# Performance work log

Measured on AMD Instinct MI355X. Metric: run time of the kernel, lower is better.

## Reference

```python
import jax, jax.numpy as jnp
import numpy as np

D_MODEL = 1024
N_HEADS = 16
D_HIDDEN = 4096
EPS = 1e-6
SCALE = float(np.sqrt(D_MODEL // N_HEADS))


def setup_inputs() -> dict:
    key = jax.random.key(0)
    ks = jax.random.split(key, 12)
    d, h = D_MODEL, D_HIDDEN
    init = lambda k, shape, fan_in: jax.random.uniform(k, shape, jnp.float32, -1.0, 1.0) / np.sqrt(fan_in)
    return {
        "x": jax.random.normal(ks[0], (2, 2048, d), jnp.float32),
        "W_q": init(ks[1], (d, d), d),
        "W_k": init(ks[2], (d, d), d),
        "W_v": init(ks[3], (d, d), d),
        "W_o": init(ks[4], (d, d), d),
        "b_o": init(ks[5], (d,), d),
        "attn_norm_w": 1.0 + jax.random.normal(ks[6], (d,), jnp.float32) / np.sqrt(d),
        "ffn_norm_w": 1.0 + jax.random.normal(ks[7], (d,), jnp.float32) / np.sqrt(d),
        "W_gate": init(ks[8], (d, h), d),
        "W_hidden": init(ks[9], (d, h), d),
        "W_out": init(ks[10], (h, d), h),
        "b_out": init(ks[11], (d,), h),
    }


def rmsnorm(x, w):
    return w * x * jax.lax.rsqrt(jnp.mean(x * x, axis=-1, keepdims=True) + EPS)


def attention(x, W_q, W_k, W_v, W_o, b_o):
    b, l, d = x.shape
    hd = d // N_HEADS
    split = lambda t: t.reshape(b, l, N_HEADS, hd).transpose(0, 2, 1, 3)  # b n l d
    q = split(x @ W_q)
    k = split(x @ W_k)
    v = split(x @ W_v)
    scores = jnp.einsum('bnld,bnmd->bnlm', q, k) / SCALE
    attn = jax.nn.softmax(scores, axis=-1)
    out = jnp.einsum('bnlm,bnmd->bnld', attn, v)
    out = out.transpose(0, 2, 1, 3).reshape(b, l, d)
    return out @ W_o + b_o


def swiglu(x, W_gate, W_hidden, W_out, b_out):
    return (jax.nn.silu(x @ W_gate) * (x @ W_hidden)) @ W_out + b_out


def reference(x, W_q, W_k, W_v, W_o, b_o, attn_norm_w, ffn_norm_w, W_gate, W_hidden, W_out, b_out):
    x = x + attention(rmsnorm(x, attn_norm_w), W_q, W_k, W_v, W_o, b_o)
    return x + swiglu(rmsnorm(x, ffn_norm_w), W_gate, W_hidden, W_out, b_out)
```

## Files before the change

kernel.cpp:

```cpp
#include <hip/hip_runtime.h>
#include <stdint.h>
#include <stddef.h>

typedef unsigned short ushort_t;
typedef __attribute__((ext_vector_type(8))) unsigned short us8;
typedef __attribute__((ext_vector_type(4))) unsigned short us4;
typedef __attribute__((ext_vector_type(2))) unsigned int u32x2;
typedef __attribute__((ext_vector_type(8))) short bf16x8;
typedef __attribute__((ext_vector_type(4))) float f32x4;
typedef __attribute__((ext_vector_type(4))) float f4;

#define DM 1024
#define SEQ 2048
#define NBATCH 2
#define NHEADS 16
#define HDIM 64
#define DH 4096
#define ROWS 4096

__device__ __forceinline__ float bf2f(ushort_t u) {
  union { unsigned int i; float f; } v; v.i = ((unsigned int)u) << 16; return v.f;
}
__device__ __forceinline__ ushort_t f2bf(float f) {
  union { float f; unsigned int i; } v; v.f = f;
  unsigned int x = v.i;
  unsigned int r = (x + 0x7FFFu + ((x >> 16) & 1u)) >> 16;
  return (ushort_t)r;
}

__global__ void f32_to_bf16(const float* __restrict__ in,
                            ushort_t* __restrict__ out, int n) {
  int i = (blockIdx.x * 256 + threadIdx.x) * 4;
  if (i >= n) return;
  f4 v = *(const f4*)(in + i);
  us4 o;
#pragma unroll
  for (int j = 0; j < 4; ++j) o[j] = f2bf(v[j]);
  *(us4*)(out + i) = o;
}

__global__ void rmsnorm_kernel(const float* __restrict__ x,
                               const float* __restrict__ w,
                               ushort_t* __restrict__ y) {
  int row = blockIdx.x;
  int t = threadIdx.x;
  f4 xv = *(const f4*)(x + (size_t)row * DM + t * 4);
  float s = 0.f;
#pragma unroll
  for (int j = 0; j < 4; ++j) s += xv[j] * xv[j];
#pragma unroll
  for (int off = 32; off >= 1; off >>= 1) s += __shfl_xor(s, off);
  __shared__ float wsum[4];
  if ((t & 63) == 0) wsum[t >> 6] = s;
  __syncthreads();
  float tot = wsum[0] + wsum[1] + wsum[2] + wsum[3];
  float scale = rsqrtf(tot * (1.0f / DM) + 1e-6f);
  f4 wv = *(const f4*)(w + t * 4);
  us4 o;
#pragma unroll
  for (int j = 0; j < 4; ++j) o[j] = f2bf(xv[j] * wv[j] * scale);
  *(us4*)(y + (size_t)row * DM + t * 4) = o;
}

#define LDKP 72

template <int EPI>
__global__ __launch_bounds__(256) void gemm_nt(
    const ushort_t* __restrict__ A, const ushort_t* __restrict__ B,
    void* __restrict__ Cv, int M, int N, int K,
    const float* __restrict__ bias, const void* __restrict__ resv) {
  __shared__ __align__(16) ushort_t As[128 * LDKP];
  __shared__ __align__(16) ushort_t Bs[128 * LDKP];
  int tid = threadIdx.x;
  int l = tid & 63;
  int w = tid >> 6;
  int wm = w >> 1, wn = w & 1;
  int m0 = blockIdx.y * 128;
  int n0 = blockIdx.x * 128;
  int lr = l & 15;
  int lk = (l >> 4) * 8;
  f32x4 acc[4][4] = {};

  const ushort_t* Ag = A + (size_t)m0 * K;

  for (int kt = 0; kt < K; kt += 64) {
#pragma unroll
    for (int i = 0; i < 4; ++i) {
      int c = i * 256 + tid;
      int row = c >> 3, col8 = (c & 7) * 8;
      *(us8*)(&As[row * LDKP + col8]) =
          *(const us8*)(Ag + (size_t)row * K + kt + col8);
    }
#pragma unroll
    for (int i = 0; i < 4; ++i) {
      int c = i * 256 + tid;
      int kr = c >> 4;
      int nc = (c & 15) * 8;
      us8 v = *(const us8*)(B + (size_t)(kt + kr) * N + n0 + nc);
      int kcol = kr ^ (((nc >> 3) & 7) << 3);
#pragma unroll
      for (int j = 0; j < 8; ++j)
        Bs[(nc + j) * LDKP + kcol] = v[j];
    }
    __syncthreads();
#pragma unroll
    for (int kk = 0; kk < 2; ++kk) {
      bf16x8 a[4], b[4];
#pragma unroll
      for (int i = 0; i < 4; ++i) {
        a[i] = *(const bf16x8*)(&As[(wm * 64 + i * 16 + lr) * LDKP + kk * 32 + lk]);
        int bn = wn * 64 + i * 16 + lr;
        int bko = (kk * 32 + lk) ^ (((bn >> 3) & 7) << 3);
        b[i] = *(const bf16x8*)(&Bs[bn * LDKP + bko]);
      }
#pragma unroll
      for (int i = 0; i < 4; ++i)
#pragma unroll
        for (int j = 0; j < 4; ++j)
          acc[i][j] = __builtin_amdgcn_mfma_f32_16x16x32_bf16(a[i], b[j], acc[i][j], 0, 0, 0);
    }
    __syncthreads();
  }

  int r0 = (l >> 4) * 4;
#pragma unroll
  for (int i = 0; i < 4; ++i) {
#pragma unroll
    for (int r = 0; r < 4; ++r) {
      int grow = m0 + wm * 64 + i * 16 + r0 + r;
#pragma unroll
      for (int j = 0; j < 4; ++j) {
        int gcol = n0 + wn * 64 + j * 16 + lr;
        size_t idx = (size_t)grow * N + gcol;
        float v = acc[i][j][r];
        if (EPI == 0) {
          ((ushort_t*)Cv)[idx] = f2bf(v);
        } else if (EPI == 1) {
          float r2 = ((const float*)resv)[idx];
          ((float*)Cv)[idx] = v + bias[gcol] + r2;
        } else {
          float g = bf2f(((const ushort_t*)resv)[idx]);
          ((ushort_t*)Cv)[idx] = f2bf(v * g / (1.0f + __expf(-g)));
        }
      }
    }
  }
}

#define LDP 72

__global__ __launch_bounds__(256) void attn_mfma(
    const ushort_t* __restrict__ Qp, const ushort_t* __restrict__ Kp,
    const ushort_t* __restrict__ Vp, ushort_t* __restrict__ Op) {
  __shared__ __align__(16) ushort_t Qs[64 * LDP];
  __shared__ __align__(16) ushort_t Ks[64 * LDP];
  __shared__ __align__(16) ushort_t Vs[64 * LDP];
  __shared__ __align__(16) ushort_t Ps[4][16 * LDP];
  int tid = threadIdx.x;
  int l = tid & 63;
  int w = tid >> 6;
  int g = l >> 4;
  int q = l & 15;
  int h = blockIdx.y, b = blockIdx.z;
  int q0 = blockIdx.x * 64;
  const size_t base = (size_t)b * SEQ * DM + h * HDIM;

#pragma unroll
  for (int i = 0; i < 2; ++i) {
    int cc = i * 256 + tid;
    int row = cc >> 3, d8 = (cc & 7) * 8;
    *(us8*)(&Qs[row * LDP + d8]) =
        *(const us8*)(Qp + base + (size_t)(q0 + row) * DM + d8);
  }

  float m_run = -3.0e38f, l_run = 0.f;
  f32x4 oacc[4] = {};

  for (int kv = 0; kv < SEQ; kv += 64) {
    __syncthreads();
#pragma unroll
    for (int i = 0; i < 2; ++i) {
      int cc = i * 256 + tid;
      int row = cc >> 3, d8 = (cc & 7) * 8;
      *(us8*)(&Ks[row * LDP + d8]) =
          *(const us8*)(Kp + base + (size_t)(kv + row) * DM + d8);
      us8 vv = *(const us8*)(Vp + base + (size_t)(kv + row) * DM + d8);
      int m8 = (d8 >> 3) & 7;
      int keysw = row ^ (m8 << 3);
#pragma unroll
      for (int j = 0; j < 8; ++j)
        Vs[(d8 + j) * LDP + keysw] = vv[j];
    }
    __syncthreads();

    f32x4 sacc[4] = {};
#pragma unroll
    for (int kk = 0; kk < 2; ++kk) {
      bf16x8 qf = *(const bf16x8*)(&Qs[(w * 16 + q) * LDP + kk * 32 + g * 8]);
#pragma unroll
      for (int t = 0; t < 4; ++t) {
        bf16x8 kf = *(const bf16x8*)(&Ks[(t * 16 + q) * LDP + kk * 32 + g * 8]);
        sacc[t] = __builtin_amdgcn_mfma_f32_16x16x32_bf16(kf, qf, sacc[t], 0, 0, 0);
      }
    }

    float mt = -3.0e38f;
#pragma unroll
    for (int t = 0; t < 4; ++t)
#pragma unroll
      for (int r = 0; r < 4; ++r) mt = fmaxf(mt, sacc[t][r]);
    mt = fmaxf(mt, __shfl_xor(mt, 16));
    mt = fmaxf(mt, __shfl_xor(mt, 32));
    mt *= 0.125f;
    float m_new = fmaxf(m_run, mt);
    float alpha = __expf(m_run - m_new);
    float psum = 0.f;
#pragma unroll
    for (int t = 0; t < 4; ++t) {
      float p0 = __expf(fmaf(sacc[t][0], 0.125f, -m_new));
      float p1 = __expf(fmaf(sacc[t][1], 0.125f, -m_new));
      float p2 = __expf(fmaf(sacc[t][2], 0.125f, -m_new));
      float p3 = __expf(fmaf(sacc[t][3], 0.125f, -m_new));
      psum += (p0 + p1) + (p2 + p3);
      u32x2 d;
      d[0] = (unsigned int)f2bf(p0) | ((unsigned int)f2bf(p1) << 16);
      d[1] = (unsigned int)f2bf(p2) | ((unsigned int)f2bf(p3) << 16);
      *(u32x2*)(&Ps[w][q * LDP + t * 16 + g * 4]) = d;
    }
    m_run = m_new;
    l_run = l_run * alpha + psum;
#pragma unroll
    for (int t = 0; t < 4; ++t)
#pragma unroll
      for (int r = 0; r < 4; ++r) oacc[t][r] *= alpha;

    __asm__ volatile("s_waitcnt lgkmcnt(0)" ::: "memory");

#pragma unroll
    for (int kk = 0; kk < 2; ++kk) {
      bf16x8 pf = *(const bf16x8*)(&Ps[w][q * LDP + kk * 32 + g * 8]);
#pragma unroll
      for (int t = 0; t < 4; ++t) {
        int d = t * 16 + q;
        int keyoff = (kk * 32 + g * 8) ^ (((d >> 3) & 7) << 3);
        bf16x8 vf = *(const bf16x8*)(&Vs[d * LDP + keyoff]);
        oacc[t] = __builtin_amdgcn_mfma_f32_16x16x32_bf16(vf, pf, oacc[t], 0, 0, 0);
      }
    }
  }

  l_run += __shfl_xor(l_run, 16);
  l_run += __shfl_xor(l_run, 32);
  float inv = 1.f / l_run;
#pragma unroll
  for (int t = 0; t < 4; ++t) {
    us4 o;
#pragma unroll
    for (int r = 0; r < 4; ++r) o[r] = f2bf(oacc[t][r] * inv);
    *(us4*)(Op + base + (size_t)(q0 + w * 16 + q) * DM + t * 16 + g * 4) = o;
  }
}

extern "C" void kernel_launch(void* const* d_in, const int* in_sizes, int n_in,
                              void* d_out, int out_size, void* d_ws, size_t ws_size,
                              hipStream_t stream) {
  const float* x   = (const float*)d_in[0];
  const float* Wq  = (const float*)d_in[1];
  const float* Wk  = (const float*)d_in[2];
  const float* Wv  = (const float*)d_in[3];
  const float* Wo  = (const float*)d_in[4];
  const float* bo  = (const float*)d_in[5];
  const float* anw = (const float*)d_in[6];
  const float* fnw = (const float*)d_in[7];
  const float* Wg  = (const float*)d_in[8];
  const float* Wh  = (const float*)d_in[9];
  const float* Wu  = (const float*)d_in[10];
  const float* bu  = (const float*)d_in[11];

  char* wsb = (char*)d_ws;
  ushort_t* Wqb = (ushort_t*)(wsb + 0);
  ushort_t* Wkb = (ushort_t*)(wsb + (2u << 20));
  ushort_t* Wvb = (ushort_t*)(wsb + (4u << 20));
  ushort_t* Wob = (ushort_t*)(wsb + (6u << 20));
  ushort_t* Wgb = (ushort_t*)(wsb + (8u << 20));
  ushort_t* Whb = (ushort_t*)(wsb + (16u << 20));
  ushort_t* Wub = (ushort_t*)(wsb + (24u << 20));
  ushort_t* hb  = (ushort_t*)(wsb + (32u << 20));
  ushort_t* qb  = (ushort_t*)(wsb + (40u << 20));
  ushort_t* kb  = (ushort_t*)(wsb + (48u << 20));
  ushort_t* vb  = (ushort_t*)(wsb + (56u << 20));
  ushort_t* ab  = (ushort_t*)(wsb + (64u << 20));
  ushort_t* gb  = (ushort_t*)(wsb + (40u << 20));
  float* out = (float*)d_out;

  f32_to_bf16<<<1024, 256, 0, stream>>>(Wq, Wqb, DM * DM);
  f32_to_bf16<<<1024, 256, 0, stream>>>(Wk, Wkb, DM * DM);
  f32_to_bf16<<<1024, 256, 0, stream>>>(Wv, Wvb, DM * DM);
  f32_to_bf16<<<1024, 256, 0, stream>>>(Wo, Wob, DM * DM);
  f32_to_bf16<<<4096, 256, 0, stream>>>(Wg, Wgb, DM * DH);
  f32_to_bf16<<<4096, 256, 0, stream>>>(Wh, Whb, DM * DH);
  f32_to_bf16<<<4096, 256, 0, stream>>>(Wu, Wub, DH * DM);

  rmsnorm_kernel<<<ROWS, 256, 0, stream>>>(x, anw, hb);
  gemm_nt<0><<<dim3(8, 32), 256, 0, stream>>>(hb, Wqb, qb, ROWS, DM, DM, nullptr, nullptr);
  gemm_nt<0><<<dim3(8, 32), 256, 0, stream>>>(hb, Wkb, kb, ROWS, DM, DM, nullptr, nullptr);
  gemm_nt<0><<<dim3(8, 32), 256, 0, stream>>>(hb, Wvb, vb, ROWS, DM, DM, nullptr, nullptr);
  attn_mfma<<<dim3(SEQ / 64, NHEADS, NBATCH), 256, 0, stream>>>(qb, kb, vb, ab);
  gemm_nt<1><<<dim3(8, 32), 256, 0, stream>>>(ab, Wob, out, ROWS, DM, DM, bo, x);

  rmsnorm_kernel<<<ROWS, 256, 0, stream>>>(out, fnw, hb);
  gemm_nt<0><<<dim3(32, 32), 256, 0, stream>>>(hb, Wgb, gb, ROWS, DH, DM, nullptr, nullptr);
  gemm_nt<2><<<dim3(32, 32), 256, 0, stream>>>(hb, Whb, gb, ROWS, DH, DM, nullptr, gb);
  gemm_nt<1><<<dim3(8, 32), 256, 0, stream>>>(gb, Wub, out, ROWS, DM, DH, bu, out);
}
```

Baseline: 535.7 us.

## Pre-transpose weights to bf16 K-major, fuse QKV GEMM, use direct global-to-LDS loads

Weight conversion now also transposes each matrix so B is stored N×K, which removes the per-element scattered LDS stores and swizzle from the GEMM's B-tile load. The GEMM fills both A and B tiles with global_load_lds 16-byte transfers into an unpadded 64-wide LDS layout. Q, K and V projections are fused into one GEMM over a concatenated weight, and attention reads the interleaved output through stride parameters. The unpadded LDS rows with no swizzle may introduce bank conflicts on the MFMA operand reads.

```diff
diff --git a/kernel.cpp b/kernel.cpp
--- a/kernel.cpp
+++ b/kernel.cpp
@@ -28,15 +28,31 @@
   return (ushort_t)r;
 }
 
-__global__ void f32_to_bf16(const float* __restrict__ in,
-                            ushort_t* __restrict__ out, int n) {
-  int i = (blockIdx.x * 256 + threadIdx.x) * 4;
-  if (i >= n) return;
-  f4 v = *(const f4*)(in + i);
-  us4 o;
-#pragma unroll
-  for (int j = 0; j < 4; ++j) o[j] = f2bf(v[j]);
-  *(us4*)(out + i) = o;
+__global__ void transpose_f32_bf16(const float* __restrict__ in,
+                                   ushort_t* __restrict__ out, int R, int C) {
+  __shared__ ushort_t tile[64][68];
+  int t = threadIdx.x;
+  int c0 = blockIdx.x * 64, r0 = blockIdx.y * 64;
+#pragma unroll
+  for (int i = 0; i < 4; ++i) {
+    int c = i * 256 + t;
+    int row = c >> 4;
+    int col4 = (c & 15) * 4;
+    f4 v = *(const f4*)(in + (size_t)(r0 + row) * C + c0 + col4);
+#pragma unroll
+    for (int j = 0; j < 4; ++j) tile[row][col4 + j] = f2bf(v[j]);
+  }
+  __syncthreads();
+#pragma unroll
+  for (int i = 0; i < 4; ++i) {
+    int c = i * 256 + t;
+    int orow = c >> 4;
+    int col4 = (c & 15) * 4;
+    us4 v;
+#pragma unroll
+    for (int j = 0; j < 4; ++j) v[j] = tile[col4 + j][orow];
+    *(us4*)(out + (size_t)(c0 + orow) * R + r0 + col4) = v;
+  }
 }
 
 __global__ void rmsnorm_kernel(const float* __restrict__ x,
@@ -62,45 +78,35 @@
   *(us4*)(y + (size_t)row * DM + t * 4) = o;
 }
 
-#define LDKP 72
-
 template <int EPI>
-__global__ __launch_bounds__(256) void gemm_nt(
-    const ushort_t* __restrict__ A, const ushort_t* __restrict__ B,
+__global__ __launch_bounds__(256) void gemm_bt(
+    const ushort_t* __restrict__ A, const ushort_t* __restrict__ Bt,
     void* __restrict__ Cv, int M, int N, int K,
     const float* __restrict__ bias, const void* __restrict__ resv) {
-  __shared__ __align__(16) ushort_t As[128 * LDKP];
-  __shared__ __align__(16) ushort_t Bs[128 * LDKP];
+  __shared__ __align__(16) ushort_t As[128 * 64];
+  __shared__ __align__(16) ushort_t Bs[128 * 64];
   int tid = threadIdx.x;
-  int l = tid & 63;
-  int w = tid >> 6;
+  int l = tid & 63, w = tid >> 6;
   int wm = w >> 1, wn = w & 1;
-  int m0 = blockIdx.y * 128;
-  int n0 = blockIdx.x * 128;
-  int lr = l & 15;
-  int lk = (l >> 4) * 8;
+  int m0 = blockIdx.y * 128, n0 = blockIdx.x * 128;
+  int lr = l & 15, lk = (l >> 4) * 8;
   f32x4 acc[4][4] = {};
-
   const ushort_t* Ag = A + (size_t)m0 * K;
+  const ushort_t* Bg = Bt + (size_t)n0 * K;
+  int srow = tid >> 3;
+  int scol = (tid & 7) * 8;
 
   for (int kt = 0; kt < K; kt += 64) {
 #pragma unroll
     for (int i = 0; i < 4; ++i) {
+      int r2 = i * 32 + srow;
       int c = i * 256 + tid;
-      int row = c >> 3, col8 = (c & 7) * 8;
-      *(us8*)(&As[row * LDKP + col8]) =
-          *(const us8*)(Ag + (size_t)row * K + kt + col8);
-    }
-#pragma unroll
-    for (int i = 0; i < 4; ++i) {
-      int c = i * 256 + tid;
-      int kr = c >> 4;
-      int nc = (c & 15) * 8;
-      us8 v = *(const us8*)(B + (size_t)(kt + kr) * N + n0 + nc);
-      int kcol = kr ^ (((nc >> 3) & 7) << 3);
-#pragma unroll
-      for (int j = 0; j < 8; ++j)
-        Bs[(nc + j) * LDKP + kcol] = v[j];
+      __builtin_amdgcn_global_load_lds(
+          (const __attribute__((address_space(1))) unsigned int*)(Ag + (size_t)r2 * K + kt + scol),
+          (__attribute__((address_space(3))) unsigned int*)(&As[c * 8]), 16, 0, 0);
+      __builtin_amdgcn_global_load_lds(
+          (const __attribute__((address_space(1))) unsigned int*)(Bg + (size_t)r2 * K + kt + scol),
+          (__attribute__((address_space(3))) unsigned int*)(&Bs[c * 8]), 16, 0, 0);
     }
     __syncthreads();
 #pragma unroll
@@ -108,10 +114,8 @@
       bf16x8 a[4], b[4];
 #pragma unroll
       for (int i = 0; i < 4; ++i) {
-        a[i] = *(const bf16x8*)(&As[(wm * 64 + i * 16 + lr) * LDKP + kk * 32 + lk]);
-        int bn = wn * 64 + i * 16 + lr;
-        int bko = (kk * 32 + lk) ^ (((bn >> 3) & 7) << 3);
-        b[i] = *(const bf16x8*)(&Bs[bn * LDKP + bko]);
+        a[i] = *(const bf16x8*)(&As[(wm * 64 + i * 16 + lr) * 64 + kk * 32 + lk]);
+        b[i] = *(const bf16x8*)(&Bs[(wn * 64 + i * 16 + lr) * 64 + kk * 32 + lk]);
       }
 #pragma unroll
       for (int i = 0; i < 4; ++i)
@@ -151,7 +155,8 @@
 
 __global__ __launch_bounds__(256) void attn_mfma(
     const ushort_t* __restrict__ Qp, const ushort_t* __restrict__ Kp,
-    const ushort_t* __restrict__ Vp, ushort_t* __restrict__ Op) {
+    const ushort_t* __restrict__ Vp, ushort_t* __restrict__ Op,
+    int qs, int os) {
   __shared__ __align__(16) ushort_t Qs[64 * LDP];
   __shared__ __align__(16) ushort_t Ks[64 * LDP];
   __shared__ __align__(16) ushort_t Vs[64 * LDP];
@@ -163,14 +168,15 @@
   int q = l & 15;
   int h = blockIdx.y, b = blockIdx.z;
   int q0 = blockIdx.x * 64;
-  const size_t base = (size_t)b * SEQ * DM + h * HDIM;
+  const size_t base = (size_t)b * SEQ * qs + h * HDIM;
+  const size_t obase = (size_t)b * SEQ * os + h * HDIM;
 
 #pragma unroll
   for (int i = 0; i < 2; ++i) {
     int cc = i * 256 + tid;
     int row = cc >> 3, d8 = (cc & 7) * 8;
     *(us8*)(&Qs[row * LDP + d8]) =
-        *(const us8*)(Qp + base + (size_t)(q0 + row) * DM + d8);
+        *(const us8*)(Qp + base + (size_t)(q0 + row) * qs + d8);
   }
 
   float m_run = -3.0e38f, l_run = 0.f;
@@ -183,8 +189,8 @@
       int cc = i * 256 + tid;
       int row = cc >> 3, d8 = (cc & 7) * 8;
       *(us8*)(&Ks[row * LDP + d8]) =
-          *(const us8*)(Kp + base + (size_t)(kv + row) * DM + d8);
-      us8 vv = *(const us8*)(Vp + base + (size_t)(kv + row) * DM + d8);
+          *(const us8*)(Kp + base + (size_t)(kv + row) * qs + d8);
+      us8 vv = *(const us8*)(Vp + base + (size_t)(kv + row) * qs + d8);
       int m8 = (d8 >> 3) & 7;
       int keysw = row ^ (m8 << 3);
 #pragma unroll
@@ -257,7 +263,7 @@
     us4 o;
 #pragma unroll
     for (int r = 0; r < 4; ++r) o[r] = f2bf(oacc[t][r] * inv);
-    *(us4*)(Op + base + (size_t)(q0 + w * 16 + q) * DM + t * 16 + g * 4) = o;
+    *(us4*)(Op + obase + (size_t)(q0 + w * 16 + q) * os + t * 16 + g * 4) = o;
   }
 }
 
@@ -278,38 +284,33 @@
   const float* bu  = (const float*)d_in[11];
 
   char* wsb = (char*)d_ws;
-  ushort_t* Wqb = (ushort_t*)(wsb + 0);
-  ushort_t* Wkb = (ushort_t*)(wsb + (2u << 20));
-  ushort_t* Wvb = (ushort_t*)(wsb + (4u << 20));
-  ushort_t* Wob = (ushort_t*)(wsb + (6u << 20));
-  ushort_t* Wgb = (ushort_t*)(wsb + (8u << 20));
-  ushort_t* Whb = (ushort_t*)(wsb + (16u << 20));
-  ushort_t* Wub = (ushort_t*)(wsb + (24u << 20));
-  ushort_t* hb  = (ushort_t*)(wsb + (32u << 20));
-  ushort_t* qb  = (ushort_t*)(wsb + (40u << 20));
-  ushort_t* kb  = (ushort_t*)(wsb + (48u << 20));
-  ushort_t* vb  = (ushort_t*)(wsb + (56u << 20));
-  ushort_t* ab  = (ushort_t*)(wsb + (64u << 20));
-  ushort_t* gb  = (ushort_t*)(wsb + (40u << 20));
+  ushort_t* WqkvT = (ushort_t*)(wsb + 0);
+  ushort_t* WoT   = (ushort_t*)(wsb + (6u << 20));
+  ushort_t* WgT   = (ushort_t*)(wsb + (8u << 20));
+  ushort_t* WhT   = (ushort_t*)(wsb + (16u << 20));
+  ushort_t* WuT   = (ushort_t*)(wsb + (24u << 20));
+  ushort_t* hb    = (ushort_t*)(wsb + (32u << 20));
+  ushort_t* qkvb  = (ushort_t*)(wsb + (40u << 20));
+  ushort_t* ab    = (ushort_t*)(wsb + (64u << 20));
+  ushort_t* gb    = (ushort_t*)(wsb + (40u << 20));
   float* out = (float*)d_out;
 
-  f32_to_bf16<<<1024, 256, 0, stream>>>(Wq, Wqb, DM * DM);
-  f32_to_bf16<<<1024, 256, 0, stream>>>(Wk, Wkb, DM * DM);
-  f32_to_bf16<<<1024, 256, 0, stream>>>(Wv, Wvb, DM * DM);
-  f32_to_bf16<<<1024, 256, 0, stream>>>(Wo, Wob, DM * DM);
-  f32_to_bf16<<<4096, 256, 0, stream>>>(Wg, Wgb, DM * DH);
-  f32_to_bf16<<<4096, 256, 0, stream>>>(Wh, Whb, DM * DH);
-  f32_to_bf16<<<4096, 256, 0, stream>>>(Wu, Wub, DH * DM);
+  transpose_f32_bf16<<<dim3(16, 16), 256, 0, stream>>>(Wq, WqkvT, DM, DM);
+  transpose_f32_bf16<<<dim3(16, 16), 256, 0, stream>>>(Wk, WqkvT + DM * DM, DM, DM);
+  transpose_f32_bf16<<<dim3(16, 16), 256, 0, stream>>>(Wv, WqkvT + 2 * DM * DM, DM, DM);
+  transpose_f32_bf16<<<dim3(16, 16), 256, 0, stream>>>(Wo, WoT, DM, DM);
+  transpose_f32_bf16<<<dim3(64, 16), 256, 0, stream>>>(Wg, WgT, DM, DH);
+  transpose_f32_bf16<<<dim3(64, 16), 256, 0, stream>>>(Wh, WhT, DM, DH);
+  transpose_f32_bf16<<<dim3(16, 64), 256, 0, stream>>>(Wu, WuT, DH, DM);
 
   rmsnorm_kernel<<<ROWS, 256, 0, stream>>>(x, anw, hb);
-  gemm_nt<0><<<dim3(8, 32), 256, 0, stream>>>(hb, Wqb, qb, ROWS, DM, DM, nullptr, nullptr);
-  gemm_nt<0><<<dim3(8, 32), 256, 0, stream>>>(hb, Wkb, kb, ROWS, DM, DM, nullptr, nullptr);
-  gemm_nt<0><<<dim3(8, 32), 256, 0, stream>>>(hb, Wvb, vb, ROWS, DM, DM, nullptr, nullptr);
-  attn_mfma<<<dim3(SEQ / 64, NHEADS, NBATCH), 256, 0, stream>>>(qb, kb, vb, ab);
-  gemm_nt<1><<<dim3(8, 32), 256, 0, stream>>>(ab, Wob, out, ROWS, DM, DM, bo, x);
+  gemm_bt<0><<<dim3(24, 32), 256, 0, stream>>>(hb, WqkvT, qkvb, ROWS, 3 * DM, DM, nullptr, nullptr);
+  attn_mfma<<<dim3(SEQ / 64, NHEADS, NBATCH), 256, 0, stream>>>(
+      qkvb, qkvb + DM, qkvb + 2 * DM, ab, 3 * DM, DM);
+  gemm_bt<1><<<dim3(8, 32), 256, 0, stream>>>(ab, WoT, out, ROWS, DM, DM, bo, x);
 
   rmsnorm_kernel<<<ROWS, 256, 0, stream>>>(out, fnw, hb);
-  gemm_nt<0><<<dim3(32, 32), 256, 0, stream>>>(hb, Wgb, gb, ROWS, DH, DM, nullptr, nullptr);
-  gemm_nt<2><<<dim3(32, 32), 256, 0, stream>>>(hb, Whb, gb, ROWS, DH, DM, nullptr, gb);
-  gemm_nt<1><<<dim3(8, 32), 256, 0, stream>>>(gb, Wub, out, ROWS, DM, DH, bu, out);
-}
+  gemm_bt<0><<<dim3(32, 32), 256, 0, stream>>>(hb, WgT, gb, ROWS, DH, DM, nullptr, nullptr);
+  gemm_bt<2><<<dim3(32, 32), 256, 0, stream>>>(hb, WhT, gb, ROWS, DH, DM, nullptr, gb);
+  gemm_bt<1><<<dim3(8, 32), 256, 0, stream>>>(gb, WuT, out, ROWS, DM, DH, bu, out);
+}
```

Result: faster. 509.1 us (-5.0%).
